# Kernel tuning notes

Hardware: AMD Instinct MI355X
Metric: run time of the kernel (lower is better)

Reference implementation:

```python
import jax, jax.numpy as jnp
import numpy as np

H = 1024   # hidden_size
D = 80     # input_dim (mel bins)
T = 512    # seq_len / target_len
B = 64     # batch


def _lstm_params(key, scale):
    k1, k2, k3, k4, k5 = jax.random.split(key, 5)
    return dict(
        W_ih=jax.random.uniform(k1, (4 * H, D), jnp.float32, -scale, scale),
        W_hh=jax.random.uniform(k2, (4 * H, H), jnp.float32, -scale, scale),
        b=jax.random.uniform(k3, (4 * H,), jnp.float32, -scale, scale),  # b_ih + b_hh fused
        W_out=jax.random.uniform(k4, (D, H), jnp.float32, -scale, scale),
        b_out=jax.random.uniform(k5, (D,), jnp.float32, -scale, scale),
    )


def setup_inputs() -> dict:
    key = jax.random.key(0)
    ks = jax.random.split(key, 8)
    scale = 1.0 / np.sqrt(H)
    fwd = _lstm_params(ks[0], scale)
    bwd = _lstm_params(ks[1], scale)
    return {
        "input_tensor": jax.random.normal(ks[2], (T, B, H), jnp.float32),
        "target_tensor": jax.random.normal(ks[3], (T, B, D), jnp.float32),
        "W_in": jax.random.uniform(ks[4], (D, H), jnp.float32, -scale, scale),
        "b_in": jax.random.uniform(ks[5], (D,), jnp.float32, -scale, scale),
        "fW_ih": fwd["W_ih"], "fW_hh": fwd["W_hh"], "fb": fwd["b"],
        "fW_out": fwd["W_out"], "fb_out": fwd["b_out"],
        "bW_ih": bwd["W_ih"], "bW_hh": bwd["W_hh"], "bb": bwd["b"],
        "bW_out": bwd["W_out"], "bb_out": bwd["b_out"],
        "target_len": T,
    }


def _run_decoder(xs, W_ih, W_hh, b, W_out, b_out):
    # xs: [T, B, D] teacher-forced inputs; PyTorch LSTM gate order i, f, g, o
    Bsz = xs.shape[1]
    h0 = jnp.zeros((Bsz, H), xs.dtype)
    c0 = jnp.zeros((Bsz, H), xs.dtype)

    def step(carry, x):
        h, c = carry
        gates = x @ W_ih.T + h @ W_hh.T + b           # [B, 4H]
        i, f, g, o = jnp.split(gates, 4, axis=-1)
        c = jax.nn.sigmoid(f) * c + jax.nn.sigmoid(i) * jnp.tanh(g)
        h = jax.nn.sigmoid(o) * jnp.tanh(c)
        y = h @ W_out.T + b_out                        # [B, D]
        return (h, c), y

    _, ys = jax.lax.scan(step, (h0, c0), xs)
    return ys  # [T, B, D]


def reference(input_tensor, target_tensor, W_in, b_in,
              fW_ih, fW_hh, fb, fW_out, fb_out,
              bW_ih, bW_hh, bb, bW_out, bb_out, target_len):
    # decoder_in projection; only the last frame is ever used as the seed input
    x0 = input_tensor[-1] @ W_in.T + b_in              # [B, D]
    # teacher-forced input stream: [x0, target[0], ..., target[T-2]]
    xs = jnp.concatenate([x0[None], target_tensor[:target_len - 1]], axis=0)
    fwd_out = _run_decoder(xs, fW_ih, fW_hh, fb, fW_out, fb_out)
    bwd_out = _run_decoder(xs, bW_ih, bW_hh, bb, bW_out, bb_out)
    return jnp.stack([fwd_out, bwd_out])               # [2, T, B, D]
```

## Files before the change

kernel.cpp:

```cpp
#include <hip/hip_runtime.h>
#include <hip/hip_bf16.h>
#include <cstdint>
#include <cstddef>

#define H   1024
#define D   80
#define DP  96
#define T   512
#define B   64
#define NG  32
#define KP  1032
#define KPI 104

typedef __attribute__((ext_vector_type(8))) short bf16x8;
typedef __attribute__((ext_vector_type(4))) float f32x4;

#define HBUF_ELEMS ((size_t)2 * (T + 1) * B * H)
#define HBUF_BYTES (HBUF_ELEMS * 2)
#define XS_ELEMS   ((size_t)T * B * DP)
#define XS_BYTES   (XS_ELEMS * 2)
#define WOUT_ELEMS ((size_t)2 * D * H)
#define WOUT_BYTES (WOUT_ELEMS * 2)
#define NFLAG      256

__device__ __forceinline__ unsigned short f2bf(float x) {
    unsigned int u = __float_as_uint(x);
    unsigned int r = (u + 0x7FFFu + ((u >> 16) & 1u)) >> 16;
    return (unsigned short)r;
}

__device__ __forceinline__ float fast_tanh(float x) {
    return 2.f / (1.f + __expf(-2.f * x)) - 1.f;
}

__device__ __forceinline__ void coh_store8(unsigned long long* p, unsigned long long v) {
    __hip_atomic_store(p, v, __ATOMIC_RELAXED, __HIP_MEMORY_SCOPE_AGENT);
}

__global__ void prep_x0(const float* __restrict__ inp, const float* __restrict__ Win,
                        const float* __restrict__ bin, unsigned short* __restrict__ xs)
{
    int o = blockIdx.x;
    int b = o / D, d = o % D;
    int lane = threadIdx.x;
    const float* irow = inp + ((size_t)(T - 1) * B + b) * H;
    const float* wrow = Win + (size_t)d * H;
    float s = 0.f;
    for (int k = lane; k < H; k += 64) s += irow[k] * wrow[k];
    for (int off = 32; off > 0; off >>= 1) s += __shfl_down(s, off, 64);
    if (lane == 0) xs[b * DP + d] = f2bf(s + bin[d]);
}

__global__ void prep_xs(const float* __restrict__ tgt, unsigned short* __restrict__ xs)
{
    int idx = blockIdx.x * 256 + threadIdx.x;
    if (idx >= T * B * DP) return;
    int t = idx / (B * DP);
    int r = idx % (B * DP);
    int b = r / DP, d = r % DP;
    if (d >= D) { xs[idx] = 0; return; }
    if (t == 0) return;
    xs[idx] = f2bf(tgt[((size_t)(t - 1) * B + b) * D + d]);
}

__global__ void prep_misc(const float* __restrict__ fWout, const float* __restrict__ bWout,
                          unsigned short* __restrict__ woutbf, unsigned short* __restrict__ hbuf,
                          unsigned int* __restrict__ flags)
{
    int idx = blockIdx.x * 256 + threadIdx.x;
    const int NW = 2 * D * H;
    const int NZ = 2 * B * H;
    if (idx < NW) {
        int dec = idx / (D * H); int rr = idx % (D * H);
        woutbf[idx] = f2bf((dec ? bWout : fWout)[rr]);
    } else if (idx < NW + NZ) {
        int z = idx - NW;
        int dec = z / (B * H); int rr = z % (B * H);
        hbuf[(size_t)dec * (T + 1) * B * H + rr] = 0;
    } else if (idx < NW + NZ + NFLAG) {
        flags[idx - NW - NZ] = 0;
    }
}

__global__ void __launch_bounds__(256, 1)
lstm_main(unsigned short* __restrict__ hbuf,
          const unsigned short* __restrict__ xs,
          const unsigned short* __restrict__ woutbf,
          unsigned int* __restrict__ flags,
          const float* __restrict__ fWih, const float* __restrict__ fWhh, const float* __restrict__ fbias,
          const float* __restrict__ bWih, const float* __restrict__ bWhh, const float* __restrict__ bbias,
          const float* __restrict__ fbout, const float* __restrict__ bbout,
          float* __restrict__ out)
{
    const int bid  = blockIdx.x;
    const int dec  = bid >> 7;
    const int blk  = bid & 127;
    const int u0   = blk << 3;
    const int tid  = threadIdx.x;
    const int wave = tid >> 6;
    const int lane = tid & 63;
    const int l15  = lane & 15;
    const int quad = lane >> 4;
    const int koff = quad * 8;

    __shared__ unsigned short sWhh[NG][KP];
    __shared__ unsigned short sWih[NG][KPI];
    __shared__ float sBias[NG];
    __shared__ float sG[B][33];
    __shared__ float sC[B][8];
    __shared__ bf16x8 sH[B];

    const float* Wih  = dec ? bWih  : fWih;
    const float* Whh  = dec ? bWhh  : fWhh;
    const float* bias = dec ? bbias : fbias;

    for (int e = tid; e < NG * H; e += 256) {
        int n = e >> 10, k = e & (H - 1);
        int row = (n >> 3) * H + u0 + (n & 7);
        sWhh[n][k] = f2bf(Whh[(size_t)row * H + k]);
    }
    for (int e = tid; e < NG * KPI; e += 256) {
        int n = e / KPI, dd = e % KPI;
        int row = (n >> 3) * H + u0 + (n & 7);
        sWih[n][dd] = (dd < D) ? f2bf(Wih[(size_t)row * D + dd]) : 0;
    }
    if (tid < NG) {
        int row = (tid >> 3) * H + u0 + (tid & 7);
        sBias[tid] = bias[row];
    }
    for (int e = tid; e < B * 8; e += 256) sC[e >> 3][e & 7] = 0.f;
    __syncthreads();

    const int m = wave * 16 + l15;
    unsigned int* myflag = flags + bid;
    const unsigned long long* pw = (const unsigned long long*)(flags + dec * 128);

    for (int t = 0; t < T; ++t) {
        f32x4 acc0e = {0.f,0.f,0.f,0.f}, acc0o = {0.f,0.f,0.f,0.f};
        f32x4 acc1e = {0.f,0.f,0.f,0.f}, acc1o = {0.f,0.f,0.f,0.f};

        const unsigned short* xrow = xs + ((size_t)t * B + m) * DP;
        #pragma unroll
        for (int kb = 0; kb < DP / 32; ++kb) {
            bf16x8 a  = *(const bf16x8*)(xrow + kb * 32 + koff);
            bf16x8 b0 = *(const bf16x8*)(&sWih[l15][kb * 32 + koff]);
            bf16x8 b1 = *(const bf16x8*)(&sWih[16 + l15][kb * 32 + koff]);
            acc0e = __builtin_amdgcn_mfma_f32_16x16x32_bf16(a, b0, acc0e, 0, 0, 0);
            acc1e = __builtin_amdgcn_mfma_f32_16x16x32_bf16(a, b1, acc1e, 0, 0, 0);
        }

        if (t > 0) {
            if (wave == 0) {
                const unsigned need = (unsigned)t;
                for (;;) {
                    unsigned long long w = __hip_atomic_load(&pw[lane], __ATOMIC_RELAXED,
                                                             __HIP_MEMORY_SCOPE_AGENT);
                    unsigned lo = (unsigned)w, hi = (unsigned)(w >> 32);
                    if (__all((lo >= need) && (hi >= need))) break;
                }
            }
            __syncthreads();
        }

        {
            const unsigned short* hrow =
                hbuf + ((size_t)(dec * (T + 1) + t) * B + m) * H + koff;
            bf16x8 A[32];
            #pragma unroll
            for (int kb = 0; kb < 32; ++kb)
                A[kb] = *(const bf16x8*)(hrow + kb * 32);
            __builtin_amdgcn_sched_barrier(0);
            #pragma unroll
            for (int kb = 0; kb < 32; kb += 2) {
                bf16x8 b0a = *(const bf16x8*)(&sWhh[l15][kb * 32 + koff]);
                bf16x8 b1a = *(const bf16x8*)(&sWhh[16 + l15][kb * 32 + koff]);
                bf16x8 b0b = *(const bf16x8*)(&sWhh[l15][(kb + 1) * 32 + koff]);
                bf16x8 b1b = *(const bf16x8*)(&sWhh[16 + l15][(kb + 1) * 32 + koff]);
                acc0e = __builtin_amdgcn_mfma_f32_16x16x32_bf16(A[kb],     b0a, acc0e, 0, 0, 0);
                acc1e = __builtin_amdgcn_mfma_f32_16x16x32_bf16(A[kb],     b1a, acc1e, 0, 0, 0);
                acc0o = __builtin_amdgcn_mfma_f32_16x16x32_bf16(A[kb + 1], b0b, acc0o, 0, 0, 0);
                acc1o = __builtin_amdgcn_mfma_f32_16x16x32_bf16(A[kb + 1], b1b, acc1o, 0, 0, 0);
            }
        }
        f32x4 acc0 = acc0e + acc0o;
        f32x4 acc1 = acc1e + acc1o;
        #pragma unroll
        for (int r = 0; r < 4; ++r) {
            sG[wave * 16 + quad * 4 + r][l15]      = acc0[r];
            sG[wave * 16 + quad * 4 + r][16 + l15] = acc1[r];
        }
        __syncthreads();

        #pragma unroll
        for (int p = tid; p < B * 8; p += 256) {
            int b = p >> 3, j = p & 7;
            float gi = sG[b][j]      + sBias[j];
            float gf = sG[b][8 + j]  + sBias[8 + j];
            float gg = sG[b][16 + j] + sBias[16 + j];
            float go = sG[b][24 + j] + sBias[24 + j];
            float i_ = 1.f / (1.f + __expf(-gi));
            float f_ = 1.f / (1.f + __expf(-gf));
            float g_ = fast_tanh(gg);
            float o_ = 1.f / (1.f + __expf(-go));
            float c  = f_ * sC[b][j] + i_ * g_;
            sC[b][j] = c;
            ((unsigned short*)&sH[b])[j] = f2bf(o_ * fast_tanh(c));
        }
        __syncthreads();

        if (tid < 64) {
            const unsigned long long* src = (const unsigned long long*)&sH[tid];
            unsigned long long v0 = src[0], v1 = src[1];
            unsigned long long* dst = (unsigned long long*)
                (hbuf + ((size_t)(dec * (T + 1) + t + 1) * B + tid) * H + u0);
            coh_store8(dst, v0);
            coh_store8(dst + 1, v1);
            asm volatile("s_waitcnt vmcnt(0)" ::: "memory");
            if (lane == 0) {
                __hip_atomic_store(myflag, (unsigned)(t + 1), __ATOMIC_RELAXED,
                                   __HIP_MEMORY_SCOPE_AGENT);
            }
        }
    }

    {
        if (wave == 0) {
            const unsigned needT = (unsigned)T;
            const unsigned long long* aw = (const unsigned long long*)flags;
            for (;;) {
                unsigned long long w0 = __hip_atomic_load(&aw[lane],      __ATOMIC_RELAXED, __HIP_MEMORY_SCOPE_AGENT);
                unsigned long long w1 = __hip_atomic_load(&aw[64 + lane], __ATOMIC_RELAXED, __HIP_MEMORY_SCOPE_AGENT);
                bool ok = ((unsigned)w0 >= needT) && ((unsigned)(w0 >> 32) >= needT) &&
                          ((unsigned)w1 >= needT) && ((unsigned)(w1 >> 32) >= needT);
                if (__all(ok)) break;
            }
            __builtin_amdgcn_fence(__ATOMIC_ACQUIRE, "agent");
        }
        __syncthreads();
    }

    for (int qq = 0; qq < 4; ++qq) {
        int q    = bid * 4 + qq;
        int ydec = q >> 9;
        int yt   = q & 511;
        const float* bout = ydec ? bbout : fbout;
        const unsigned short* hr = hbuf + ((size_t)(ydec * (T + 1) + yt + 1) * B + m) * H;
        const unsigned short* wb = woutbf + (size_t)ydec * D * H;

        bf16x8 Ah[32];
        #pragma unroll
        for (int kb = 0; kb < 32; ++kb)
            Ah[kb] = *(const bf16x8*)(hr + kb * 32 + koff);
        __builtin_amdgcn_sched_barrier(0);

        #pragma unroll
        for (int nt = 0; nt < 5; ++nt) {
            f32x4 acc = {0.f, 0.f, 0.f, 0.f};
            const unsigned short* wrow = wb + (size_t)(nt * 16 + l15) * H;
            #pragma unroll 8
            for (int kb = 0; kb < H / 32; ++kb) {
                bf16x8 bf = *(const bf16x8*)(wrow + kb * 32 + koff);
                acc = __builtin_amdgcn_mfma_f32_16x16x32_bf16(Ah[kb], bf, acc, 0, 0, 0);
            }
            float bo = bout[nt * 16 + l15];
            #pragma unroll
            for (int r = 0; r < 4; ++r) {
                int bb_ = wave * 16 + quad * 4 + r;
                out[((size_t)(ydec * T + yt) * B + bb_) * D + nt * 16 + l15] = acc[r] + bo;
            }
        }
    }
}

extern "C" void kernel_launch(void* const* d_in, const int* in_sizes, int n_in,
                              void* d_out, int out_size, void* d_ws, size_t ws_size,
                              hipStream_t stream)
{
    const float* input  = (const float*)d_in[0];
    const float* target = (const float*)d_in[1];
    const float* Win    = (const float*)d_in[2];
    const float* bin    = (const float*)d_in[3];
    const float* fWih   = (const float*)d_in[4];
    const float* fWhh   = (const float*)d_in[5];
    const float* fb     = (const float*)d_in[6];
    const float* fWout  = (const float*)d_in[7];
    const float* fbout  = (const float*)d_in[8];
    const float* bWih   = (const float*)d_in[9];
    const float* bWhh   = (const float*)d_in[10];
    const float* bb     = (const float*)d_in[11];
    const float* bWout  = (const float*)d_in[12];
    const float* bbout  = (const float*)d_in[13];
    float* out = (float*)d_out;

    unsigned short* hbuf  = (unsigned short*)d_ws;
    unsigned short* xsb   = (unsigned short*)((char*)d_ws + HBUF_BYTES);
    unsigned short* wout  = (unsigned short*)((char*)d_ws + HBUF_BYTES + XS_BYTES);
    unsigned int*   flags = (unsigned int*)((char*)d_ws + HBUF_BYTES + XS_BYTES + WOUT_BYTES);

    prep_x0<<<B * D, 64, 0, stream>>>(input, Win, bin, xsb);
    prep_xs<<<(T * B * DP + 255) / 256, 256, 0, stream>>>(target, xsb);
    {
        int n = 2 * D * H + 2 * B * H + NFLAG;
        prep_misc<<<(n + 255) / 256, 256, 0, stream>>>(fWout, bWout, wout, hbuf, flags);
    }

    void* args[] = { &hbuf, &xsb, &wout, &flags,
                     (void*)&fWih, (void*)&fWhh, (void*)&fb,
                     (void*)&bWih, (void*)&bWhh, (void*)&bb,
                     (void*)&fbout, (void*)&bbout, &out };
    hipLaunchCooperativeKernel((void*)lstm_main, dim3(256), dim3(256), args, 0, stream);
}
```

Measured before the change: 3.745 ms.

## Replace per-step flag barrier with sentinel-polled hidden-state data readiness

```diff
diff --git a/kernel.cpp b/kernel.cpp
--- a/kernel.cpp
+++ b/kernel.cpp
@@ -14,6 +14,9 @@
 
 typedef __attribute__((ext_vector_type(8))) short bf16x8;
 typedef __attribute__((ext_vector_type(4))) float f32x4;
+typedef __attribute__((ext_vector_type(4))) unsigned int u32x4;
+
+#define SENT64 0x7F807F807F807F80ull
 
 #define HBUF_ELEMS ((size_t)2 * (T + 1) * B * H)
 #define HBUF_BYTES (HBUF_ELEMS * 2)
@@ -35,6 +38,9 @@
 
 __device__ __forceinline__ void coh_store8(unsigned long long* p, unsigned long long v) {
     __hip_atomic_store(p, v, __ATOMIC_RELAXED, __HIP_MEMORY_SCOPE_AGENT);
+}
+__device__ __forceinline__ unsigned long long coh_load8(const unsigned long long* p) {
+    return __hip_atomic_load(p, __ATOMIC_RELAXED, __HIP_MEMORY_SCOPE_AGENT);
 }
 
 __global__ void prep_x0(const float* __restrict__ inp, const float* __restrict__ Win,
@@ -61,6 +67,17 @@
     if (d >= D) { xs[idx] = 0; return; }
     if (t == 0) return;
     xs[idx] = f2bf(tgt[((size_t)(t - 1) * B + b) * D + d]);
+}
+
+__global__ void prep_sent(u32x4* __restrict__ hbuf16)
+{
+    const size_t perdec = (size_t)T * B * H / 8;
+    const u32x4 s4 = {0x7F807F80u, 0x7F807F80u, 0x7F807F80u, 0x7F807F80u};
+    for (size_t p = (size_t)blockIdx.x * 256 + threadIdx.x;
+         p < 2 * perdec; p += (size_t)gridDim.x * 256) {
+        size_t dec = p / perdec, r = p % perdec;
+        hbuf16[(dec * (T + 1) + 1) * (B * H / 8) + r] = s4;
+    }
 }
 
 __global__ void prep_misc(const float* __restrict__ fWout, const float* __restrict__ bWout,
@@ -133,7 +150,8 @@
 
     const int m = wave * 16 + l15;
     unsigned int* myflag = flags + bid;
-    const unsigned long long* pw = (const unsigned long long*)(flags + dec * 128);
+
+    union FragU { unsigned long long q[2]; bf16x8 v; };
 
     for (int t = 0; t < T; ++t) {
         f32x4 acc0e = {0.f,0.f,0.f,0.f}, acc0o = {0.f,0.f,0.f,0.f};
@@ -149,38 +167,36 @@
             acc1e = __builtin_amdgcn_mfma_f32_16x16x32_bf16(a, b1, acc1e, 0, 0, 0);
         }
 
-        if (t > 0) {
-            if (wave == 0) {
-                const unsigned need = (unsigned)t;
-                for (;;) {
-                    unsigned long long w = __hip_atomic_load(&pw[lane], __ATOMIC_RELAXED,
-                                                             __HIP_MEMORY_SCOPE_AGENT);
-                    unsigned lo = (unsigned)w, hi = (unsigned)(w >> 32);
-                    if (__all((lo >= need) && (hi >= need))) break;
+        FragU A[32];
+        {
+            const unsigned long long* hq = (const unsigned long long*)
+                (hbuf + ((size_t)(dec * (T + 1) + t) * B + m) * H + koff);
+            for (;;) {
+                #pragma unroll
+                for (int kb = 0; kb < 32; ++kb) {
+                    A[kb].q[0] = coh_load8(hq + kb * 8);
+                    A[kb].q[1] = coh_load8(hq + kb * 8 + 1);
                 }
+                bool ok = true;
+                #pragma unroll
+                for (int kb = 0; kb < 32; ++kb)
+                    ok = ok && (A[kb].q[0] != SENT64) && (A[kb].q[1] != SENT64);
+                if (__all(ok)) break;
+                __builtin_amdgcn_s_sleep(1);
             }
-            __syncthreads();
-        }
-
-        {
-            const unsigned short* hrow =
-                hbuf + ((size_t)(dec * (T + 1) + t) * B + m) * H + koff;
-            bf16x8 A[32];
-            #pragma unroll
-            for (int kb = 0; kb < 32; ++kb)
-                A[kb] = *(const bf16x8*)(hrow + kb * 32);
-            __builtin_amdgcn_sched_barrier(0);
-            #pragma unroll
-            for (int kb = 0; kb < 32; kb += 2) {
-                bf16x8 b0a = *(const bf16x8*)(&sWhh[l15][kb * 32 + koff]);
-                bf16x8 b1a = *(const bf16x8*)(&sWhh[16 + l15][kb * 32 + koff]);
-                bf16x8 b0b = *(const bf16x8*)(&sWhh[l15][(kb + 1) * 32 + koff]);
-                bf16x8 b1b = *(const bf16x8*)(&sWhh[16 + l15][(kb + 1) * 32 + koff]);
-                acc0e = __builtin_amdgcn_mfma_f32_16x16x32_bf16(A[kb],     b0a, acc0e, 0, 0, 0);
-                acc1e = __builtin_amdgcn_mfma_f32_16x16x32_bf16(A[kb],     b1a, acc1e, 0, 0, 0);
-                acc0o = __builtin_amdgcn_mfma_f32_16x16x32_bf16(A[kb + 1], b0b, acc0o, 0, 0, 0);
-                acc1o = __builtin_amdgcn_mfma_f32_16x16x32_bf16(A[kb + 1], b1b, acc1o, 0, 0, 0);
-            }
+        }
+        __builtin_amdgcn_sched_barrier(0);
+
+        #pragma unroll
+        for (int kb = 0; kb < 32; kb += 2) {
+            bf16x8 b0a = *(const bf16x8*)(&sWhh[l15][kb * 32 + koff]);
+            bf16x8 b1a = *(const bf16x8*)(&sWhh[16 + l15][kb * 32 + koff]);
+            bf16x8 b0b = *(const bf16x8*)(&sWhh[l15][(kb + 1) * 32 + koff]);
+            bf16x8 b1b = *(const bf16x8*)(&sWhh[16 + l15][(kb + 1) * 32 + koff]);
+            acc0e = __builtin_amdgcn_mfma_f32_16x16x32_bf16(A[kb].v,     b0a, acc0e, 0, 0, 0);
+            acc1e = __builtin_amdgcn_mfma_f32_16x16x32_bf16(A[kb].v,     b1a, acc1e, 0, 0, 0);
+            acc0o = __builtin_amdgcn_mfma_f32_16x16x32_bf16(A[kb + 1].v, b0b, acc0o, 0, 0, 0);
+            acc1o = __builtin_amdgcn_mfma_f32_16x16x32_bf16(A[kb + 1].v, b1b, acc1o, 0, 0, 0);
         }
         f32x4 acc0 = acc0e + acc0o;
         f32x4 acc1 = acc1e + acc1o;
@@ -215,11 +231,14 @@
                 (hbuf + ((size_t)(dec * (T + 1) + t + 1) * B + tid) * H + u0);
             coh_store8(dst, v0);
             coh_store8(dst + 1, v1);
-            asm volatile("s_waitcnt vmcnt(0)" ::: "memory");
-            if (lane == 0) {
-                __hip_atomic_store(myflag, (unsigned)(t + 1), __ATOMIC_RELAXED,
-                                   __HIP_MEMORY_SCOPE_AGENT);
-            }
+        }
+    }
+
+    if (tid < 64) {
+        asm volatile("s_waitcnt vmcnt(0)" ::: "memory");
+        if (lane == 0) {
+            __hip_atomic_store(myflag, (unsigned)T, __ATOMIC_RELAXED,
+                               __HIP_MEMORY_SCOPE_AGENT);
         }
     }
 
@@ -233,6 +252,7 @@
                 bool ok = ((unsigned)w0 >= needT) && ((unsigned)(w0 >> 32) >= needT) &&
                           ((unsigned)w1 >= needT) && ((unsigned)(w1 >> 32) >= needT);
                 if (__all(ok)) break;
+                __builtin_amdgcn_s_sleep(1);
             }
             __builtin_amdgcn_fence(__ATOMIC_ACQUIRE, "agent");
         }
@@ -299,6 +319,7 @@
 
     prep_x0<<<B * D, 64, 0, stream>>>(input, Win, bin, xsb);
     prep_xs<<<(T * B * DP + 255) / 256, 256, 0, stream>>>(target, xsb);
+    prep_sent<<<4096, 256, 0, stream>>>((u32x4*)hbuf);
     {
         int n = 2 * D * H + 2 * B * H + NFLAG;
         prep_misc<<<(n + 255) / 256, 256, 0, stream>>>(fWout, bWout, wout, hbuf, flags);
```

Measured after the change: 7.075 ms. 88.9% more time.
